# Performance work log

Hardware: AMD Instinct MI355X
Metric: run time of the kernel (lower is better)

The kernel has to match this reference:

```python
import jax, jax.numpy as jnp
import numpy as np
import math


def _ln(x, g, b):
    mu = jnp.mean(x, -1, keepdims=True)
    var = jnp.mean((x - mu) ** 2, -1, keepdims=True)
    return (x - mu) / jnp.sqrt(var + 1e-5) * g + b


def _gelu(x):
    # torch nn.GELU default = exact erf form
    return jax.nn.gelu(x, approximate=False)


def _prm_exp(x, w):
    # FAVOR+ positive random features: exp(w x - |x|^2/2) / sqrt(m)
    m = w.shape[0]
    xd = jnp.sum(x * x, axis=-1, keepdims=True) * 0.5  # (B,T,1)
    wtx = jnp.einsum('btd,md->btm', x, w)
    return jnp.exp(wtx - xd) / math.sqrt(m)


def setup_inputs() -> dict:
    key = jax.random.key(0)
    ks = jax.random.split(key, 8)
    B, T = 16, 3136
    Cin, D = 768, 384
    m = int(D * 0.5)  # kernel_ratio = 0.5 -> 192 random features
    s = lambda fan_in: 1.0 / np.sqrt(fan_in)
    inp = {
        'input_1': jax.random.normal(ks[0], (B, T, Cin // 2), jnp.float32),
        'input_2': jax.random.normal(ks[1], (B, T, Cin // 2), jnp.float32),
        'W1': jax.random.uniform(ks[2], (Cin, D), jnp.float32, -s(Cin), s(Cin)),
        'b1': jnp.zeros((D,), jnp.float32),
        'W2': jax.random.uniform(ks[3], (D, D), jnp.float32, -s(D), s(D)),
        'b2': jnp.zeros((D,), jnp.float32),
        'kqv_w': jax.random.uniform(ks[4], (D, 3 * D), jnp.float32, -s(D), s(D)),
        'kqv_b': jnp.zeros((3 * D,), jnp.float32),
        'proj_w': jax.random.uniform(ks[5], (D, D), jnp.float32, -s(D), s(D)),
        'proj_b': jnp.zeros((D,), jnp.float32),
        'ln1_g': jnp.ones((D,), jnp.float32),
        'ln1_b': jnp.zeros((D,), jnp.float32),
        'ln2_g': jnp.ones((D,), jnp.float32),
        'ln2_b': jnp.zeros((D,), jnp.float32),
        'mlp_w1': jax.random.uniform(ks[6], (D, D), jnp.float32, -s(D), s(D)),
        'mlp_b1': jnp.zeros((D,), jnp.float32),
        'mlp_w2': jax.random.uniform(ks[7], (D, D), jnp.float32, -s(D), s(D)),
        'mlp_b2': jnp.zeros((D,), jnp.float32),
    }
    # frozen orthogonal projection (m, D) scaled by sqrt(m), as in Token_performer
    g = np.random.default_rng(0).standard_normal((D, m)).astype(np.float32)
    q, _ = np.linalg.qr(g)  # (D, m) orthonormal columns
    inp['w_prm'] = jnp.asarray((q.T * math.sqrt(m)).astype(np.float32))  # (m, D)
    return inp


def reference(input_1, input_2, W1, b1, W2, b2, kqv_w, kqv_b, proj_w, proj_b,
              ln1_g, ln1_b, ln2_g, ln2_b, mlp_w1, mlp_b1, mlp_w2, mlp_b2, w_prm):
    # concatFuse: Linear -> GELU -> Linear
    x = jnp.concatenate([input_1, input_2], axis=2)
    x = _gelu(x @ W1 + b1) @ W2 + b2  # (B, T, D)

    # Token_performer (dropout = identity in eval)
    xn = _ln(x, ln1_g, ln1_b)
    kqv = xn @ kqv_w + kqv_b
    k, q, v = jnp.split(kqv, 3, axis=-1)  # torch.split order: k, q, v
    kp = _prm_exp(k, w_prm)  # (B, T, m)
    qp = _prm_exp(q, w_prm)  # (B, T, m)
    Dn = jnp.einsum('btm,bm->bt', qp, kp.sum(axis=1))[..., None]  # (B, T, 1)
    kptv = jnp.einsum('btd,btm->bdm', v, kp)  # (B, D, m)
    y = jnp.einsum('btm,bdm->btd', qp, kptv) / (Dn + 1e-8)  # (B, T, D)
    y = v + (y @ proj_w + proj_b)  # residual is v, per Token_performer

    z = _ln(y, ln2_g, ln2_b)
    h = _gelu(z @ mlp_w1 + mlp_b1) @ mlp_w2 + mlp_b2
    return y + h
```

## Files before the change

### kernel.cpp

```cpp
#include <hip/hip_runtime.h>
#include <math.h>

typedef unsigned short u16;
typedef unsigned int   u32;
typedef __attribute__((ext_vector_type(8))) short short8;
typedef __attribute__((ext_vector_type(4))) float f32x4;

typedef const void __attribute__((address_space(1))) gvoid_t;
typedef void       __attribute__((address_space(3))) svoid_t;

__device__ __forceinline__ void gload_lds16(const void* g, void* l){
    __builtin_amdgcn_global_load_lds((gvoid_t*)g, (svoid_t*)l, 16, 0, 0);
}

__device__ __forceinline__ float gelu_f(float x){
    return 0.5f * x * (1.0f + erff(x * 0.70710678118654752f));
}
__device__ __forceinline__ u16 f2b(float x){
    union{float f; u32 u;} v; v.f = x;
    u32 r = (v.u + 0x7fffu + ((v.u >> 16) & 1u)) >> 16;
    return (u16)r;
}
__device__ __forceinline__ float b2f(u16 h){
    union{u32 u; float f;} v; v.u = ((u32)h) << 16; return v.f;
}

template<int EPI, int GUARD, int CGUARD, int MINW>
__global__ __launch_bounds__(256, MINW)
void gemm_bf16(const u16* __restrict__ A, int lda,
               const u16* __restrict__ B, int ldb,
               void* __restrict__ Cv, int ldc,
               const float* __restrict__ bias,
               const float* __restrict__ rowv,
               void* __restrict__ resid, int ldr,
               int Mrows, int Ncols, int K, int splitK,
               long sA, long sB, long sC, long sRV,
               float scale)
{
    const int bz = blockIdx.z;
    const int b  = bz / splitK, kc = bz % splitK;
    A += (long)b * sA;  B += (long)b * sB;
    const float* rv = (EPI == 3) ? rowv + (long)b * sRV : nullptr;

    __shared__ u16 SMEM[16384];
    __shared__ float xds[128];
    u16* const As = SMEM;
    u16* const Bs = SMEM + 8192;

    const int tid = threadIdx.x;

    const int gx  = gridDim.x;
    const int nwg = gx * gridDim.y;
    const int L   = blockIdx.y * gx + blockIdx.x;
    const int q8  = nwg >> 3, r8 = nwg & 7;
    const int xc  = L & 7,   i8 = L >> 3;
    const int nid = (xc < r8 ? xc * (q8 + 1) : r8 * (q8 + 1) + (xc - r8) * q8) + i8;
    const int row0 = (nid / gx) * 128, col0 = (nid % gx) * 128;

    f32x4 acc[4][4] = {};
    float sqacc[4] = {0.f, 0.f, 0.f, 0.f};

    const int l  = tid & 63, w4 = tid >> 6;
    const int wr = w4 >> 1, wc = w4 & 1;
    const int g  = l >> 4,  mr = l & 15;

    const int kLen   = K / splitK;
    const int kStart = kc * kLen;
    const int nt     = kLen / 64;

    const int m0   = w4 * 8 + (l >> 3);
    const int k8s  = (l & 7) ^ (m0 & 7);
    const int lBase = w4 * 512 + l * 8;
    const u16* gA0 = A + (long)(row0 + m0) * lda + kStart + k8s * 8;
    const u16* gB0 = B + (long)(col0 + m0) * ldb + kStart + k8s * 8;

    int aOff[4], bOff[4], sl[2];
    #pragma unroll
    for (int i = 0; i < 4; i++){
        aOff[i] = (wr * 64 + i * 16 + mr) * 64;
        bOff[i] = (wc * 64 + i * 16 + mr) * 64;
    }
    #pragma unroll
    for (int kk = 0; kk < 2; kk++)
        sl[kk] = (((kk * 4 + g) ^ (mr & 7)) & 7) * 8;

    for (int t = 0; t < nt; t++){
        __syncthreads();
        #pragma unroll
        for (int q = 0; q < 4; q++){
            gload_lds16(gA0 + (long)q * 32 * lda + t * 64, &As[lBase + q * 2048]);
            gload_lds16(gB0 + (long)q * 32 * ldb + t * 64, &Bs[lBase + q * 2048]);
        }
        __syncthreads();

        short8 af[2][4], bfr[2][4];
        #pragma unroll
        for (int kk = 0; kk < 2; kk++)
            #pragma unroll
            for (int i = 0; i < 4; i++){
                af[kk][i]  = *(const short8*)&As[aOff[i] + sl[kk]];
                bfr[kk][i] = *(const short8*)&Bs[bOff[i] + sl[kk]];
            }
        if (EPI == 10){
            #pragma unroll
            for (int kk = 0; kk < 2; kk++)
                #pragma unroll
                for (int i = 0; i < 4; i++)
                    #pragma unroll
                    for (int e = 0; e < 8; e++){
                        float f_ = b2f((u16)af[kk][i][e]);
                        sqacc[i] += f_ * f_;
                    }
        }
        #pragma unroll
        for (int kk = 0; kk < 2; kk++)
            #pragma unroll
            for (int i = 0; i < 4; i++)
                #pragma unroll
                for (int j = 0; j < 4; j++)
                    acc[i][j] = __builtin_amdgcn_mfma_f32_16x16x32_bf16(af[kk][i], bfr[kk][j], acc[i][j], 0, 0, 0);
    }

    if (EPI == 10){
        #pragma unroll
        for (int i = 0; i < 4; i++){
            float s = sqacc[i];
            s += __shfl_xor(s, 16);
            s += __shfl_xor(s, 32);
            if (l < 16) xds[wr * 64 + i * 16 + l] = 0.5f * s;
        }
    }
    __syncthreads();

    float* Cf = (float*)Cv + (long)b * sC;
    u16*   Cb = (u16*)Cv   + (EPI == 10 ? 0L : (EPI == 8 ? (long)bz : (long)b) * sC);

    if (EPI == 10 && bz == 0){
        #pragma unroll
        for (int i = 0; i < 4; i++){
            #pragma unroll
            for (int j = 0; j < 4; j++){
                const int col = col0 + wc * 64 + j * 16 + mr;
                if (CGUARD && col >= Ncols) continue;
                const int lrow = wr * 64 + i * 16 + g * 4;
                u16 pk[4];
                #pragma unroll
                for (int r = 0; r < 4; r++)
                    pk[r] = f2b(expf(acc[i][j][r] - xds[lrow + r]) * scale);
                *(ushort4*)&Cb[(long)col * ldc + row0 + lrow] = *(ushort4*)pk;
            }
        }
        return;
    }

    if (EPI == 9){
        #pragma unroll
        for (int i = 0; i < 4; i++){
            #pragma unroll
            for (int j = 0; j < 4; j++){
                const int col = col0 + wc * 64 + j * 16 + mr;
                if (CGUARD && col >= Ncols) continue;
                const float bv = bias[col];
                #pragma unroll
                for (int r = 0; r < 4; r++){
                    const int row = row0 + wr * 64 + i * 16 + g * 4 + r;
                    if (GUARD && row >= Mrows) continue;
                    const float vv = acc[i][j][r] + bv
                        + b2f(((const u16*)resid)[(long)row * ldr + col]);
                    Cf[(long)row * ldc + col] = vv;
                }
            }
        }
        return;
    }

    #pragma unroll
    for (int i = 0; i < 4; i++){
        #pragma unroll
        for (int j = 0; j < 4; j++){
            const int cl = wc * 64 + j * 16 + mr;
            const float bv = (EPI == 0 || EPI == 1 || EPI == 11 || EPI == 12)
                           ? bias[col0 + cl] : 0.f;
            u16 pk[4];
            #pragma unroll
            for (int r = 0; r < 4; r++){
                const int rl = wr * 64 + i * 16 + g * 4 + r;
                float vv = acc[i][j][r];
                if      (EPI == 1)  vv = gelu_f(vv + bv);
                else if (EPI == 3)  vv = vv / (rv[row0 + rl] + 1e-8f);
                else if (EPI == 10) vv = expf(vv - xds[rl]) * scale;
                else                vv += bv;
                pk[r] = f2b(vv);
                SMEM[rl * 128 + cl] = pk[r];
            }
            if (EPI == 12 && col0 >= 768){
                const int lrow = wr * 64 + i * 16 + g * 4;
                u16* vt = (u16*)resid;
                *(ushort4*)&vt[(long)(col0 + cl - 768) * ldr + row0 + lrow] = *(ushort4*)pk;
            }
        }
    }
    __syncthreads();

    u16* dst; long ld;
    if (EPI == 10){ dst = (u16*)resid; ld = ldr; }
    else          { dst = Cb;          ld = ldc; }
    #pragma unroll
    for (int s = 0; s < 8; s++){
        const int oi = s * 256 + tid;
        const int rl = oi >> 4, c8 = (oi & 15) << 3;
        const int row = row0 + rl, col = col0 + c8;
        if (GUARD && row >= Mrows) continue;
        if (CGUARD && col >= Ncols) continue;
        uint4 pv = *(uint4*)&SMEM[rl * 128 + c8];
        if (EPI == 11){
            const u16* rp = (const u16*)resid + (long)row * ldr + col;
            uint4 rv4 = *(const uint4*)rp;
            u16* a = (u16*)&pv; const u16* c = (const u16*)&rv4;
            #pragma unroll
            for (int e = 0; e < 8; e++) a[e] = f2b(b2f(a[e]) + b2f(c[e]));
        }
        *(uint4*)&dst[(long)row * ld + col] = pv;
    }
}

template<int INF32>
__global__ __launch_bounds__(256)
void ln_kernel(const void* __restrict__ xv, u16* __restrict__ ob,
               const float* __restrict__ g, const float* __restrict__ bta)
{
    const int lane = threadIdx.x & 63;
    const long r = (long)blockIdx.x * 4 + (threadIdx.x >> 6);
    float v[6]; float s = 0.f;
    #pragma unroll
    for (int i = 0; i < 6; i++){
        const int c = lane + i * 64;
        v[i] = INF32 ? ((const float*)xv)[r * 384 + c]
                     : b2f(((const u16*)xv)[r * 384 + c]);
        s += v[i];
    }
    #pragma unroll
    for (int off = 32; off; off >>= 1) s += __shfl_xor(s, off);
    const float mu = s * (1.0f/384.0f);
    float q = 0.f;
    #pragma unroll
    for (int i = 0; i < 6; i++){ float d = v[i] - mu; q += d*d; }
    #pragma unroll
    for (int off = 32; off; off >>= 1) q += __shfl_xor(q, off);
    const float inv = rsqrtf(q * (1.0f/384.0f) + 1e-5f);
    #pragma unroll
    for (int i = 0; i < 6; i++){
        const int c = lane + i*64;
        ob[r * 384 + c] = f2b((v[i] - mu) * inv * g[c] + bta[c]);
    }
}

__global__ __launch_bounds__(256)
void dn_kernel(const u16* __restrict__ qp, const float* __restrict__ kpsum,
               float* __restrict__ Dn, int T)
{
    const int lane = threadIdx.x & 63;
    const long r = (long)blockIdx.x * 4 + (threadIdx.x >> 6);
    const int b = (int)(r / T);
    const u16* qr = qp + r * 192;
    const float* ks = kpsum + (long)b * 192;
    float s = 0.f;
    #pragma unroll
    for (int i = 0; i < 3; i++){ const int m = lane + i*64; s += b2f(qr[m]) * ks[m]; }
    #pragma unroll
    for (int off = 32; off; off >>= 1) s += __shfl_xor(s, off);
    if (lane == 0) Dn[r] = s;
}

__global__ __launch_bounds__(256)
void kpsum2_kernel(const u16* __restrict__ kpT, float* __restrict__ kpsum, long Mc, int T)
{
    const int lane = threadIdx.x & 63;
    const int gw = blockIdx.x * 4 + (threadIdx.x >> 6);
    const int m = gw % 192, bl = gw / 192;
    const u16* row = kpT + (long)m * Mc + (long)bl * T;
    float s = 0.f;
    for (int i = lane; i < T; i += 64) s += b2f(row[i]);
    #pragma unroll
    for (int off = 32; off; off >>= 1) s += __shfl_xor(s, off);
    if (lane == 0) kpsum[bl * 192 + m] = s;
}

__global__ __launch_bounds__(256)
void zero_kernel(float* __restrict__ p, long n)
{
    long i = (long)blockIdx.x * 256 + threadIdx.x;
    long stride = (long)gridDim.x * 256;
    for (; i < n; i += stride) p[i] = 0.f;
}

__global__ __launch_bounds__(256)
void ca_kernel(const float* __restrict__ i1, const float* __restrict__ i2,
               u16* __restrict__ a0, long nquad)
{
    long idx = (long)blockIdx.x * 256 + threadIdx.x;
    if (idx >= nquad) return;
    const long r = idx / 192;
    const int  c0 = (int)(idx % 192) * 4;
    const float* src = (c0 < 384) ? &i1[r * 384 + c0] : &i2[r * 384 + (c0 - 384)];
    float4 v = *(const float4*)src;
    u32 w0 = (u32)f2b(v.x) | ((u32)f2b(v.y) << 16);
    u32 w1 = (u32)f2b(v.z) | ((u32)f2b(v.w) << 16);
    *(uint2*)&a0[r * 768 + c0] = make_uint2(w0, w1);
}

__global__ __launch_bounds__(256)
void wt_kernel(const float* __restrict__ w, u16* __restrict__ wt, int K, int N, long total)
{
    long idx = (long)blockIdx.x * 256 + threadIdx.x;
    if (idx >= total) return;
    const long n = idx / K, k = idx - n * K;
    wt[idx] = f2b(w[k * N + n]);
}

__global__ __launch_bounds__(256)
void cvt_kernel(const float* __restrict__ s, u16* __restrict__ d, long n4)
{
    long idx = (long)blockIdx.x * 256 + threadIdx.x;
    if (idx >= n4) return;
    float4 v = *(const float4*)&s[idx * 4];
    u32 w0 = (u32)f2b(v.x) | ((u32)f2b(v.y) << 16);
    u32 w1 = (u32)f2b(v.z) | ((u32)f2b(v.w) << 16);
    *(uint2*)&d[idx * 4] = make_uint2(w0, w1);
}

extern "C" void kernel_launch(void* const* d_in, const int* in_sizes, int n_in,
                              void* d_out, int out_size, void* d_ws, size_t ws_size,
                              hipStream_t stream)
{
    const long T = 3136;
    const float prm_scale = 0.07216878364870322f;

    const float* in1    = (const float*)d_in[0];
    const float* in2    = (const float*)d_in[1];
    const float* W1     = (const float*)d_in[2];
    const float* b1     = (const float*)d_in[3];
    const float* W2     = (const float*)d_in[4];
    const float* b2     = (const float*)d_in[5];
    const float* kqv_w  = (const float*)d_in[6];
    const float* kqv_b  = (const float*)d_in[7];
    const float* proj_w = (const float*)d_in[8];
    const float* proj_b = (const float*)d_in[9];
    const float* ln1_g  = (const float*)d_in[10];
    const float* ln1_b  = (const float*)d_in[11];
    const float* ln2_g  = (const float*)d_in[12];
    const float* ln2_b  = (const float*)d_in[13];
    const float* mlp_w1 = (const float*)d_in[14];
    const float* mlp_b1 = (const float*)d_in[15];
    const float* mlp_w2 = (const float*)d_in[16];
    const float* mlp_b2 = (const float*)d_in[17];
    const float* w_prm  = (const float*)d_in[18];
    float* out = (float*)d_out;

    char* p = (char*)d_ws;
    auto alloc = [&](long bytes)->char*{ char* r = p; p += (bytes + 255) & ~255L; return r; };

    u16* w1t   = (u16*)alloc(294912L * 2);
    u16* w2t   = (u16*)alloc(147456L * 2);
    u16* kqvt  = (u16*)alloc(442368L * 2);
    u16* prjt  = (u16*)alloc(147456L * 2);
    u16* m1t   = (u16*)alloc(147456L * 2);
    u16* m2t   = (u16*)alloc(147456L * 2);
    u16* wprmb = (u16*)alloc(256L * 384 * 2);
    char* chunkBase = p;

    const long perBatch = 2368L * T * 2 + T * 4
                        + 192L * 4 + 73728L * 2;
    const long fixed = (long)(chunkBase - (char*)d_ws) + (1L << 20);
    int nb = 2;
    for (int cand = 16; cand >= 2; cand >>= 1){
        if (fixed + (long)cand * perBatch + 128L * 1024 <= (long)ws_size){ nb = cand; break; }
    }

    const dim3 blk(256);

    wt_kernel<<<dim3((294912 + 255) / 256), blk, 0, stream>>>(W1, w1t, 768, 384, 294912);
    wt_kernel<<<dim3((147456 + 255) / 256), blk, 0, stream>>>(W2, w2t, 384, 384, 147456);
    wt_kernel<<<dim3((442368 + 255) / 256), blk, 0, stream>>>(kqv_w, kqvt, 384, 1152, 442368);
    wt_kernel<<<dim3((147456 + 255) / 256), blk, 0, stream>>>(proj_w, prjt, 384, 384, 147456);
    wt_kernel<<<dim3((147456 + 255) / 256), blk, 0, stream>>>(mlp_w1, m1t, 384, 384, 147456);
    wt_kernel<<<dim3((147456 + 255) / 256), blk, 0, stream>>>(mlp_w2, m2t, 384, 384, 147456);
    zero_kernel<<<dim3(64), blk, 0, stream>>>((float*)wprmb, 256L * 384 / 2);
    cvt_kernel<<<dim3((18432 + 255) / 256), blk, 0, stream>>>(w_prm, wprmb, 18432);

    for (int b0 = 0; b0 < 16; b0 += nb){
        const long Mc = (long)nb * T;
        const int  gy128 = (int)(Mc / 128);
        const float* i1 = in1 + (long)b0 * T * 384;
        const float* i2 = in2 + (long)b0 * T * 384;
        float* outc = out + (long)b0 * T * 384;

        p = chunkBase;
        u16*  big   = (u16*)alloc(Mc * 1152 * 2);
        u16*  xb    = (u16*)alloc(Mc * 384 * 2);
        u16*  qpb   = (u16*)alloc(Mc * 192 * 2);
        u16*  vT    = (u16*)alloc(384L * Mc * 2);
        u16*  kpT   = (u16*)alloc(256L * Mc * 2);
        float* Dn   = (float*)alloc(Mc * 4);
        float* kpsum= (float*)alloc((long)nb * 192 * 4);
        u16*  kptvb = (u16*)alloc((long)nb * 73728 * 2);
        (void)alloc(128L * 1024);

        u16* a0   = big;
        u16* h1   = big + Mc * 768;
        u16* kqvb = big;
        u16* hbuf = big;
        u16* ybf  = vT;

        {
            long nq = Mc * 192;
            ca_kernel<<<dim3((unsigned)((nq + 255) / 256)), blk, 0, stream>>>(i1, i2, a0, nq);
        }
        gemm_bf16<1,0,0,4><<<dim3(3, gy128, 1), blk, 0, stream>>>(
            a0, 768, w1t, 768, h1, 384, b1, nullptr, nullptr, 0,
            (int)Mc, 384, 768, 1, 0,0,0,0, 0.f);
        gemm_bf16<0,0,0,4><<<dim3(3, gy128, 1), blk, 0, stream>>>(
            h1, 384, w2t, 384, xb, 384, b2, nullptr, nullptr, 0,
            (int)Mc, 384, 384, 1, 0,0,0,0, 0.f);
        ln_kernel<0><<<dim3((unsigned)(Mc / 4)), blk, 0, stream>>>(xb, xb, ln1_g, ln1_b);
        gemm_bf16<12,0,0,4><<<dim3(9, gy128, 1), blk, 0, stream>>>(
            xb, 384, kqvt, 384, kqvb, 1152, kqv_b, nullptr, vT, (int)Mc,
            (int)Mc, 1152, 384, 1, 0,0,0,0, 0.f);
        gemm_bf16<10,0,1,2><<<dim3(2, gy128, 2), blk, 0, stream>>>(
            kqvb, 1152, wprmb, 384, kpT, (int)Mc, nullptr, nullptr, qpb, 192,
            (int)Mc, 192, 384, 1, 384, 0, 0, 0, prm_scale);
        kpsum2_kernel<<<dim3(nb * 48), blk, 0, stream>>>(kpT, kpsum, Mc, (int)T);
        gemm_bf16<8,0,1,4><<<dim3(2, 3, nb), blk, 0, stream>>>(
            vT, (int)Mc, kpT, (int)Mc, kptvb, 192, nullptr, nullptr, nullptr, 0,
            384, 192, 3136, 1, 3136, 3136, 73728, 0, 0.f);
        dn_kernel<<<dim3((unsigned)(Mc / 4)), blk, 0, stream>>>(qpb, kpsum, Dn, (int)T);
        gemm_bf16<3,1,0,4><<<dim3(3, 25, nb), blk, 0, stream>>>(
            qpb, 192, kptvb, 192, xb, 384, nullptr, Dn, nullptr, 0,
            (int)T, 384, 192, 1, T*192, 73728, T*384, T, 0.f);
        gemm_bf16<11,0,0,4><<<dim3(3, gy128, 1), blk, 0, stream>>>(
            xb, 384, prjt, 384, ybf, 384, proj_b, nullptr, kqvb + 768, 1152,
            (int)Mc, 384, 384, 1, 0,0,0,0, 0.f);
        ln_kernel<0><<<dim3((unsigned)(Mc / 4)), blk, 0, stream>>>(ybf, xb, ln2_g, ln2_b);
        gemm_bf16<1,0,0,4><<<dim3(3, gy128, 1), blk, 0, stream>>>(
            xb, 384, m1t, 384, hbuf, 384, mlp_b1, nullptr, nullptr, 0,
            (int)Mc, 384, 384, 1, 0,0,0,0, 0.f);
        gemm_bf16<9,0,0,4><<<dim3(3, gy128, 1), blk, 0, stream>>>(
            hbuf, 384, m2t, 384, outc, 384, mlp_b2, nullptr, ybf, 384,
            (int)Mc, 384, 384, 1, 0,0,0,0, 0.f);
    }
}
```

Baseline: 525.7 us.

## Vectorize LayerNorm and concat kernels, merge weight prep into one launch

The LayerNorm kernel now has each lane load eight bf16 values with a single 16-byte load. It computes sum and sum-of-squares in one reduction pass, where it used to make two passes, so the variance uses the E[x^2]-mu^2 form with a slight numerical risk. The concat/convert kernel packs eight values per thread and uses a grid-stride loop over a fixed grid. The eight weight transpose, zero and convert launches are merged into one prep kernel, and the last template argument of the random-feature GEMM changes from 2 to 3.

Measured after the change: 509.8 us. 1.03x faster.

```diff
diff --git a/kernel.cpp b/kernel.cpp
--- a/kernel.cpp
+++ b/kernel.cpp
@@ -224,34 +224,39 @@
     }
 }
 
-template<int INF32>
 __global__ __launch_bounds__(256)
-void ln_kernel(const void* __restrict__ xv, u16* __restrict__ ob,
-               const float* __restrict__ g, const float* __restrict__ bta)
+void ln8_kernel(const u16* __restrict__ x, u16* __restrict__ o,
+                const float* __restrict__ g, const float* __restrict__ bta)
 {
     const int lane = threadIdx.x & 63;
     const long r = (long)blockIdx.x * 4 + (threadIdx.x >> 6);
-    float v[6]; float s = 0.f;
-    #pragma unroll
-    for (int i = 0; i < 6; i++){
-        const int c = lane + i * 64;
-        v[i] = INF32 ? ((const float*)xv)[r * 384 + c]
-                     : b2f(((const u16*)xv)[r * 384 + c]);
-        s += v[i];
-    }
-    #pragma unroll
-    for (int off = 32; off; off >>= 1) s += __shfl_xor(s, off);
-    const float mu = s * (1.0f/384.0f);
-    float q = 0.f;
-    #pragma unroll
-    for (int i = 0; i < 6; i++){ float d = v[i] - mu; q += d*d; }
-    #pragma unroll
-    for (int off = 32; off; off >>= 1) q += __shfl_xor(q, off);
-    const float inv = rsqrtf(q * (1.0f/384.0f) + 1e-5f);
-    #pragma unroll
-    for (int i = 0; i < 6; i++){
-        const int c = lane + i*64;
-        ob[r * 384 + c] = f2b((v[i] - mu) * inv * g[c] + bta[c]);
+    float v[8];
+    float s = 0.f, q = 0.f;
+    if (lane < 48){
+        uint4 v4 = *(const uint4*)&x[r * 384 + lane * 8];
+        const u16* h = (const u16*)&v4;
+        #pragma unroll
+        for (int e = 0; e < 8; e++){
+            v[e] = b2f(h[e]);
+            s += v[e];
+            q += v[e] * v[e];
+        }
+    }
+    #pragma unroll
+    for (int off = 32; off; off >>= 1){
+        s += __shfl_xor(s, off);
+        q += __shfl_xor(q, off);
+    }
+    const float mu  = s * (1.0f / 384.0f);
+    const float var = q * (1.0f / 384.0f) - mu * mu;
+    const float inv = rsqrtf(var + 1e-5f);
+    if (lane < 48){
+        const int c0 = lane * 8;
+        u16 pk[8];
+        #pragma unroll
+        for (int e = 0; e < 8; e++)
+            pk[e] = f2b((v[e] - mu) * inv * g[c0 + e] + bta[c0 + e]);
+        *(uint4*)&o[r * 384 + c0] = *(uint4*)pk;
     }
 }
 
@@ -287,46 +292,57 @@
 }
 
 __global__ __launch_bounds__(256)
-void zero_kernel(float* __restrict__ p, long n)
-{
-    long i = (long)blockIdx.x * 256 + threadIdx.x;
-    long stride = (long)gridDim.x * 256;
-    for (; i < n; i += stride) p[i] = 0.f;
+void ca_kernel(const float* __restrict__ i1, const float* __restrict__ i2,
+               u16* __restrict__ a0, long n8)
+{
+    const long stride = (long)gridDim.x * 256;
+    for (long idx = (long)blockIdx.x * 256 + threadIdx.x; idx < n8; idx += stride){
+        const long r = idx / 96;
+        const int  c0 = (int)(idx % 96) * 8;
+        const float* src = (c0 < 384) ? &i1[r * 384 + c0] : &i2[r * 384 + (c0 - 384)];
+        float4 a = *(const float4*)src;
+        float4 b = *(const float4*)(src + 4);
+        uint4 pk;
+        pk.x = (u32)f2b(a.x) | ((u32)f2b(a.y) << 16);
+        pk.y = (u32)f2b(a.z) | ((u32)f2b(a.w) << 16);
+        pk.z = (u32)f2b(b.x) | ((u32)f2b(b.y) << 16);
+        pk.w = (u32)f2b(b.z) | ((u32)f2b(b.w) << 16);
+        *(uint4*)&a0[r * 768 + c0] = pk;
+    }
 }
 
 __global__ __launch_bounds__(256)
-void ca_kernel(const float* __restrict__ i1, const float* __restrict__ i2,
-               u16* __restrict__ a0, long nquad)
-{
-    long idx = (long)blockIdx.x * 256 + threadIdx.x;
-    if (idx >= nquad) return;
-    const long r = idx / 192;
-    const int  c0 = (int)(idx % 192) * 4;
-    const float* src = (c0 < 384) ? &i1[r * 384 + c0] : &i2[r * 384 + (c0 - 384)];
-    float4 v = *(const float4*)src;
-    u32 w0 = (u32)f2b(v.x) | ((u32)f2b(v.y) << 16);
-    u32 w1 = (u32)f2b(v.z) | ((u32)f2b(v.w) << 16);
-    *(uint2*)&a0[r * 768 + c0] = make_uint2(w0, w1);
-}
-
-__global__ __launch_bounds__(256)
-void wt_kernel(const float* __restrict__ w, u16* __restrict__ wt, int K, int N, long total)
-{
-    long idx = (long)blockIdx.x * 256 + threadIdx.x;
-    if (idx >= total) return;
-    const long n = idx / K, k = idx - n * K;
-    wt[idx] = f2b(w[k * N + n]);
-}
-
-__global__ __launch_bounds__(256)
-void cvt_kernel(const float* __restrict__ s, u16* __restrict__ d, long n4)
-{
-    long idx = (long)blockIdx.x * 256 + threadIdx.x;
-    if (idx >= n4) return;
-    float4 v = *(const float4*)&s[idx * 4];
-    u32 w0 = (u32)f2b(v.x) | ((u32)f2b(v.y) << 16);
-    u32 w1 = (u32)f2b(v.z) | ((u32)f2b(v.w) << 16);
-    *(uint2*)&d[idx * 4] = make_uint2(w0, w1);
+void prep_kernel(const float* __restrict__ W1, const float* __restrict__ W2,
+                 const float* __restrict__ kqv_w, const float* __restrict__ proj_w,
+                 const float* __restrict__ mlp_w1, const float* __restrict__ mlp_w2,
+                 const float* __restrict__ w_prm,
+                 u16* __restrict__ w1t, u16* __restrict__ w2t, u16* __restrict__ kqvt,
+                 u16* __restrict__ prjt, u16* __restrict__ m1t, u16* __restrict__ m2t,
+                 u16* __restrict__ wprmb)
+{
+    const long i = (long)blockIdx.x * 256 + threadIdx.x;
+    if (i < 294912){
+        const long n = i / 768, k = i - n * 768;
+        w1t[i] = f2b(W1[k * 384 + n]);
+    } else if (i < 442368){
+        const long j = i - 294912, n = j / 384, k = j - n * 384;
+        w2t[j] = f2b(W2[k * 384 + n]);
+    } else if (i < 884736){
+        const long j = i - 442368, n = j / 384, k = j - n * 384;
+        kqvt[j] = f2b(kqv_w[k * 1152 + n]);
+    } else if (i < 1032192){
+        const long j = i - 884736, n = j / 384, k = j - n * 384;
+        prjt[j] = f2b(proj_w[k * 384 + n]);
+    } else if (i < 1179648){
+        const long j = i - 1032192, n = j / 384, k = j - n * 384;
+        m1t[j] = f2b(mlp_w1[k * 384 + n]);
+    } else if (i < 1327104){
+        const long j = i - 1179648, n = j / 384, k = j - n * 384;
+        m2t[j] = f2b(mlp_w2[k * 384 + n]);
+    } else if (i < 1425408){
+        const long j = i - 1327104;
+        wprmb[j] = (j < 73728) ? f2b(w_prm[j]) : (u16)0;
+    }
 }
 
 extern "C" void kernel_launch(void* const* d_in, const int* in_sizes, int n_in,
@@ -379,14 +395,9 @@
 
     const dim3 blk(256);
 
-    wt_kernel<<<dim3((294912 + 255) / 256), blk, 0, stream>>>(W1, w1t, 768, 384, 294912);
-    wt_kernel<<<dim3((147456 + 255) / 256), blk, 0, stream>>>(W2, w2t, 384, 384, 147456);
-    wt_kernel<<<dim3((442368 + 255) / 256), blk, 0, stream>>>(kqv_w, kqvt, 384, 1152, 442368);
-    wt_kernel<<<dim3((147456 + 255) / 256), blk, 0, stream>>>(proj_w, prjt, 384, 384, 147456);
-    wt_kernel<<<dim3((147456 + 255) / 256), blk, 0, stream>>>(mlp_w1, m1t, 384, 384, 147456);
-    wt_kernel<<<dim3((147456 + 255) / 256), blk, 0, stream>>>(mlp_w2, m2t, 384, 384, 147456);
-    zero_kernel<<<dim3(64), blk, 0, stream>>>((float*)wprmb, 256L * 384 / 2);
-    cvt_kernel<<<dim3((18432 + 255) / 256), blk, 0, stream>>>(w_prm, wprmb, 18432);
+    prep_kernel<<<dim3((1425408 + 255) / 256), blk, 0, stream>>>(
+        W1, W2, kqv_w, proj_w, mlp_w1, mlp_w2, w_prm,
+        w1t, w2t, kqvt, prjt, m1t, m2t, wprmb);
 
     for (int b0 = 0; b0 < 16; b0 += nb){
         const long Mc = (long)nb * T;
@@ -412,21 +423,18 @@
         u16* hbuf = big;
         u16* ybf  = vT;
 
-        {
-            long nq = Mc * 192;
-            ca_kernel<<<dim3((unsigned)((nq + 255) / 256)), blk, 0, stream>>>(i1, i2, a0, nq);
-        }
+        ca_kernel<<<dim3(4096), blk, 0, stream>>>(i1, i2, a0, Mc * 96);
         gemm_bf16<1,0,0,4><<<dim3(3, gy128, 1), blk, 0, stream>>>(
             a0, 768, w1t, 768, h1, 384, b1, nullptr, nullptr, 0,
             (int)Mc, 384, 768, 1, 0,0,0,0, 0.f);
         gemm_bf16<0,0,0,4><<<dim3(3, gy128, 1), blk, 0, stream>>>(
             h1, 384, w2t, 384, xb, 384, b2, nullptr, nullptr, 0,
             (int)Mc, 384, 384, 1, 0,0,0,0, 0.f);
-        ln_kernel<0><<<dim3((unsigned)(Mc / 4)), blk, 0, stream>>>(xb, xb, ln1_g, ln1_b);
+        ln8_kernel<<<dim3((unsigned)(Mc / 4)), blk, 0, stream>>>(xb, xb, ln1_g, ln1_b);
         gemm_bf16<12,0,0,4><<<dim3(9, gy128, 1), blk, 0, stream>>>(
             xb, 384, kqvt, 384, kqvb, 1152, kqv_b, nullptr, vT, (int)Mc,
             (int)Mc, 1152, 384, 1, 0,0,0,0, 0.f);
-        gemm_bf16<10,0,1,2><<<dim3(2, gy128, 2), blk, 0, stream>>>(
+        gemm_bf16<10,0,1,3><<<dim3(2, gy128, 2), blk, 0, stream>>>(
             kqvb, 1152, wprmb, 384, kpT, (int)Mc, nullptr, nullptr, qpb, 192,
             (int)Mc, 192, 384, 1, 384, 0, 0, 0, prm_scale);
         kpsum2_kernel<<<dim3(nb * 48), blk, 0, stream>>>(kpT, kpsum, Mc, (int)T);
@@ -440,7 +448,7 @@
         gemm_bf16<11,0,0,4><<<dim3(3, gy128, 1), blk, 0, stream>>>(
             xb, 384, prjt, 384, ybf, 384, proj_b, nullptr, kqvb + 768, 1152,
             (int)Mc, 384, 384, 1, 0,0,0,0, 0.f);
-        ln_kernel<0><<<dim3((unsigned)(Mc / 4)), blk, 0, stream>>>(ybf, xb, ln2_g, ln2_b);
+        ln8_kernel<<<dim3((unsigned)(Mc / 4)), blk, 0, stream>>>(ybf, xb, ln2_g, ln2_b);
         gemm_bf16<1,0,0,4><<<dim3(3, gy128, 1), blk, 0, stream>>>(
             xb, 384, m1t, 384, hbuf, 384, mlp_b1, nullptr, nullptr, 0,
             (int)Mc, 384, 384, 1, 0,0,0,0, 0.f);
```
